# Kernel tuning notes

Measured on AMD Instinct MI355X. Metric: run time of the kernel, lower is better.

The kernel has to match this reference:

```python
import jax, jax.numpy as jnp
import numpy as np

N_HEAD = 12

def setup_inputs() -> dict:
    key = jax.random.key(0)
    ks = jax.random.split(key, 5)
    B, T, C = 4, 2048, 768
    x = jax.random.normal(ks[0], (B, T, C), dtype=jnp.float32)
    s_in = 1.0 / np.sqrt(C)
    W_qkv = jax.random.normal(ks[1], (C, 3 * C), dtype=jnp.float32) * s_in
    b_qkv = jnp.zeros((3 * C,), dtype=jnp.float32)
    W_proj = jax.random.normal(ks[2], (C, C), dtype=jnp.float32) * s_in
    b_proj = jnp.zeros((C,), dtype=jnp.float32)
    return {"x": x, "W_qkv": W_qkv, "b_qkv": b_qkv, "W_proj": W_proj, "b_proj": b_proj}


def reference(x, W_qkv, b_qkv, W_proj, b_proj):
    B, T, C = x.shape
    H = N_HEAD
    D = C // H  # head dim
    qkv = x @ W_qkv + b_qkv                      # [B,T,3C]
    q, k, v = jnp.split(qkv, 3, axis=-1)
    # [B,T,C] -> [B,H,T,D]
    q = q.reshape(B, T, H, D).transpose(0, 2, 1, 3)
    k = k.reshape(B, T, H, D).transpose(0, 2, 1, 3)
    v = v.reshape(B, T, H, D).transpose(0, 2, 1, 3)
    att = jnp.einsum("bhqd,bhkd->bhqk", q, k) / jnp.sqrt(jnp.asarray(D, x.dtype))
    causal = jnp.tril(jnp.ones((T, T), dtype=bool))
    att = jnp.where(causal, att, jnp.asarray(-jnp.inf, att.dtype))
    att = jax.nn.softmax(att, axis=-1)
    y = jnp.einsum("bhqk,bhkd->bhqd", att, v)    # [B,H,T,D]
    y = y.transpose(0, 2, 1, 3).reshape(B, T, C)
    return y @ W_proj + b_proj
```

## Files before the change

kernel.cpp:

```cpp
#include <hip/hip_runtime.h>
#include <hip/hip_bf16.h>

typedef __bf16 bf16x8 __attribute__((ext_vector_type(8)));
typedef float f32x4 __attribute__((ext_vector_type(4)));
typedef unsigned int u32x4 __attribute__((ext_vector_type(4)));
typedef unsigned int u32x2 __attribute__((ext_vector_type(2)));
typedef int i32x2 __attribute__((ext_vector_type(2)));
typedef unsigned short u16;
typedef unsigned long long u64;

__device__ __forceinline__ u16 f2bf(float f) {
  unsigned u = __builtin_bit_cast(unsigned, f);
  u += 0x7FFFu + ((u >> 16) & 1u);
  return (u16)(u >> 16);
}
__device__ __forceinline__ unsigned cvtpk(float a, float b) {
  float2 f; f.x = a; f.y = b;
  __hip_bfloat162 h = __float22bfloat162_rn(f);
  unsigned u;
  __builtin_memcpy(&u, &h, 4);
  return u;
}

__device__ __forceinline__ void plswap(unsigned &a, unsigned &b) {
  i32x2 r = __builtin_amdgcn_permlane32_swap((int)a, (int)b, false, false);
  a = (unsigned)r[0];
  b = (unsigned)r[1];
}

__device__ __forceinline__ void gll16(const u16* g, u16* l) {
  __builtin_amdgcn_global_load_lds(
      (const __attribute__((address_space(1))) unsigned int*)g,
      (__attribute__((address_space(3))) unsigned int*)l, 16, 0, 0);
}

__global__ void cast_x_kernel(const float* __restrict__ in, u16* __restrict__ out, int n4) {
  int i = blockIdx.x * blockDim.x + threadIdx.x;
  if (i >= n4) return;
  f32x4 v = *(const f32x4*)(in + (size_t)i * 4);
  u32x2 pk;
  pk[0] = cvtpk(v[0], v[1]);
  pk[1] = cvtpk(v[2], v[3]);
  *(u32x2*)(out + (size_t)i * 4) = pk;
}

__global__ void transpose_cast_kernel(const float* __restrict__ W, u16* __restrict__ WT, int K, int N) {
  __shared__ float tile[32][33];
  int c0 = blockIdx.x * 32, r0 = blockIdx.y * 32;
  int tx = threadIdx.x & 31, tg = threadIdx.x >> 5;
#pragma unroll
  for (int i = 0; i < 4; ++i) {
    int r = tg + i * 8;
    tile[r][tx] = W[(size_t)(r0 + r) * N + c0 + tx];
  }
  __syncthreads();
#pragma unroll
  for (int i = 0; i < 4; ++i) {
    int r = tg + i * 8;
    WT[(size_t)(c0 + r) * K + r0 + tx] = f2bf(tile[tx][r]);
  }
}

__global__ __launch_bounds__(256, 4) void gemm_qkv_kernel(
    const u16* __restrict__ A, const u16* __restrict__ BT, const float* __restrict__ bias,
    u16* __restrict__ Qb, u16* __restrict__ Kb, u16* __restrict__ Vt) {
  constexpr int K = 768;
  __shared__ u16 Asm[2][128 * 32];
  __shared__ u16 Bsm[2][128 * 32];
  const int tid = threadIdx.x;
  const int w = tid >> 6, lane = tid & 63;
  const int l15 = lane & 15, quad = lane >> 4;
  const int srow = tid >> 2, scol = (tid & 3) * 8;
  const int m0 = blockIdx.y * 128, n0 = blockIdx.x * 128;
  const u16* Ag = A + (size_t)(m0 + srow) * K + scol;
  const u16* Bg = BT + (size_t)(n0 + srow) * K + scol;
  const int mw = (w >> 1) * 64, nw = (w & 1) * 64;
  f32x4 acc[4][4];
#pragma unroll
  for (int i = 0; i < 4; ++i)
#pragma unroll
    for (int j = 0; j < 4; ++j) acc[i][j] = {0.f, 0.f, 0.f, 0.f};
  for (int k0 = 0; k0 < K; k0 += 64) {
    __syncthreads();
#pragma unroll
    for (int h = 0; h < 2; ++h)
#pragma unroll
      for (int rb = 0; rb < 2; ++rb) {
        gll16(Ag + (size_t)rb * 64 * K + k0 + h * 32, &Asm[h][(rb * 64 + w * 16) * 32]);
        gll16(Bg + (size_t)rb * 64 * K + k0 + h * 32, &Bsm[h][(rb * 64 + w * 16) * 32]);
      }
    __syncthreads();
#pragma unroll
    for (int h = 0; h < 2; ++h) {
      bf16x8 af[4], bfj[4];
#pragma unroll
      for (int i = 0; i < 4; ++i) af[i] = *(const bf16x8*)&Asm[h][(mw + i * 16 + l15) * 32 + quad * 8];
#pragma unroll
      for (int j = 0; j < 4; ++j) bfj[j] = *(const bf16x8*)&Bsm[h][(nw + j * 16 + l15) * 32 + quad * 8];
#pragma unroll
      for (int i = 0; i < 4; ++i)
#pragma unroll
        for (int j = 0; j < 4; ++j)
          acc[i][j] = __builtin_amdgcn_mfma_f32_16x16x32_bf16(af[i], bfj[j], acc[i][j], 0, 0, 0);
    }
  }
  const int sec = blockIdx.x / 6;
  const int nbase = n0 - sec * 768;
#pragma unroll
  for (int j = 0; j < 4; ++j) {
    const int nloc = nbase + nw + j * 16 + l15;
    const float bv = bias[sec * 768 + nloc];
    const int h = nloc >> 6, d = nloc & 63;
#pragma unroll
    for (int i = 0; i < 4; ++i) {
      const int m = m0 + mw + i * 16 + quad * 4;
      const int bb = m >> 11, trow = m & 2047;
      if (sec == 2) {
        u32x2 pk;
        pk[0] = cvtpk(acc[i][j][0] + bv, acc[i][j][1] + bv);
        pk[1] = cvtpk(acc[i][j][2] + bv, acc[i][j][3] + bv);
        *(u32x2*)(Vt + (size_t)((bb * 12 + h) * 64 + d) * 2048 + trow) = pk;
      } else {
        u16* dst = (sec == 0) ? Qb : Kb;
        const float scl = (sec == 0) ? 0.125f * 1.44269504f : 1.0f;
#pragma unroll
        for (int r = 0; r < 4; ++r)
          dst[(size_t)((bb * 12 + h) * 2048 + trow + r) * 64 + d] = f2bf((acc[i][j][r] + bv) * scl);
      }
    }
  }
}

__global__ __launch_bounds__(256, 4) void gemm_proj_kernel(
    const u16* __restrict__ A, const u16* __restrict__ BT, const float* __restrict__ bias,
    float* __restrict__ out) {
  constexpr int K = 768;
  __shared__ u16 Asm[2][64 * 32];
  __shared__ u16 Bsm[2][128 * 32];
  const int tid = threadIdx.x;
  const int w = tid >> 6, lane = tid & 63;
  const int l15 = lane & 15, quad = lane >> 4;
  const int srow = tid >> 2, scol = (tid & 3) * 8;
  const int m0 = blockIdx.y * 64, n0 = blockIdx.x * 128;
  const u16* Ag = A + (size_t)(m0 + srow) * K + scol;
  const u16* Bg = BT + (size_t)(n0 + srow) * K + scol;
  const int mw = (w >> 1) * 32, nw = (w & 1) * 64;
  f32x4 acc[2][4];
#pragma unroll
  for (int i = 0; i < 2; ++i)
#pragma unroll
    for (int j = 0; j < 4; ++j) acc[i][j] = {0.f, 0.f, 0.f, 0.f};
  for (int k0 = 0; k0 < K; k0 += 64) {
    __syncthreads();
#pragma unroll
    for (int h = 0; h < 2; ++h) {
      gll16(Ag + k0 + h * 32, &Asm[h][(w * 16) * 32]);
#pragma unroll
      for (int rb = 0; rb < 2; ++rb)
        gll16(Bg + (size_t)rb * 64 * K + k0 + h * 32, &Bsm[h][(rb * 64 + w * 16) * 32]);
    }
    __syncthreads();
#pragma unroll
    for (int h = 0; h < 2; ++h) {
      bf16x8 af[2], bfj[4];
#pragma unroll
      for (int i = 0; i < 2; ++i) af[i] = *(const bf16x8*)&Asm[h][(mw + i * 16 + l15) * 32 + quad * 8];
#pragma unroll
      for (int j = 0; j < 4; ++j) bfj[j] = *(const bf16x8*)&Bsm[h][(nw + j * 16 + l15) * 32 + quad * 8];
#pragma unroll
      for (int i = 0; i < 2; ++i)
#pragma unroll
        for (int j = 0; j < 4; ++j)
          acc[i][j] = __builtin_amdgcn_mfma_f32_16x16x32_bf16(af[i], bfj[j], acc[i][j], 0, 0, 0);
    }
  }
#pragma unroll
  for (int j = 0; j < 4; ++j) {
    const int n = n0 + nw + j * 16 + l15;
    const float bv = bias[n];
#pragma unroll
    for (int i = 0; i < 2; ++i) {
      const int m = m0 + mw + i * 16 + quad * 4;
#pragma unroll
      for (int r = 0; r < 4; ++r) out[(size_t)(m + r) * 768 + n] = acc[i][j][r] + bv;
    }
  }
}

__global__ __launch_bounds__(256) void attn_split_kernel(
    const u16* __restrict__ Qg, const u16* __restrict__ Kg, const u16* __restrict__ Vtg,
    u16* __restrict__ Yb, float* __restrict__ Opart, float* __restrict__ lpart) {
  constexpr int T = 2048, D = 64;
  constexpr int LDP = 72;
  constexpr float MBOUND = 20.0f;
  __shared__ u16 Ks[64 * LDP];
  __shared__ u16 VTs[64 * LDP];
  const int s = 79 - blockIdx.x;
  const int bh = blockIdx.y;
  int qt, c;
  if (s < 8) { qt = s; c = 0; }
  else if (s < 24) { qt = 8 + ((s - 8) >> 1); c = (s - 8) & 1; }
  else if (s < 48) { int u = s - 24; int q3 = u / 3; qt = 16 + q3; c = u - 3 * q3; }
  else { int u = s - 48; qt = 24 + (u >> 2); c = u & 3; }
  const int niter = min(8, qt + 1 - 8 * c);
  const int tid = threadIdx.x;
  const int w = tid >> 6, lane = tid & 63;
  const int l15 = lane & 15, quad = lane >> 4;
  const int srow = tid >> 2, scol = (tid & 3) * 16;
  const u16* Kp = Kg + (size_t)bh * T * D;
  const u16* VTp = Vtg + (size_t)bh * D * T;

  const int qq = qt * 64 + w * 16 + l15;
  const u16* qrow = Qg + ((size_t)bh * T + qq) * D;
  const bf16x8 qfa = *(const bf16x8*)(qrow + quad * 8);
  const bf16x8 qfb = *(const bf16x8*)(qrow + 32 + quad * 8);

  f32x4 o[4] = {{0,0,0,0},{0,0,0,0},{0,0,0,0},{0,0,0,0}};
  float lv = 0.f;

  int ktg = c * 8;
  u32x4 kA = *(const u32x4*)(Kp + (size_t)(ktg * 64 + srow) * D + scol);
  u32x4 kB = *(const u32x4*)(Kp + (size_t)(ktg * 64 + srow) * D + scol + 8);
  u32x4 vA = *(const u32x4*)(VTp + (size_t)srow * T + ktg * 64 + scol);
  u32x4 vB = *(const u32x4*)(VTp + (size_t)srow * T + ktg * 64 + scol + 8);

  for (int j = 0; j < niter; ++j) {
    ktg = c * 8 + j;
    __syncthreads();
    *(u32x4*)&Ks[srow * LDP + scol] = kA;
    *(u32x4*)&Ks[srow * LDP + scol + 8] = kB;
    {
      u32x2 t0; t0[0] = vA[0]; t0[1] = vA[1];
      u32x2 t1; t1[0] = vA[2]; t1[1] = vA[3];
      u32x2 t2; t2[0] = vB[0]; t2[1] = vB[1];
      u32x2 t3; t3[0] = vB[2]; t3[1] = vB[3];
      *(u32x2*)&VTs[srow * LDP + scol] = t0;
      *(u32x2*)&VTs[srow * LDP + scol + 8] = t1;
      *(u32x2*)&VTs[srow * LDP + scol + 4] = t2;
      *(u32x2*)&VTs[srow * LDP + scol + 12] = t3;
    }
    __syncthreads();
    if (j + 1 < niter) {
      const int k1 = (ktg + 1) * 64;
      kA = *(const u32x4*)(Kp + (size_t)(k1 + srow) * D + scol);
      kB = *(const u32x4*)(Kp + (size_t)(k1 + srow) * D + scol + 8);
      vA = *(const u32x4*)(VTp + (size_t)srow * T + k1 + scol);
      vB = *(const u32x4*)(VTp + (size_t)srow * T + k1 + scol + 8);
    }
    f32x4 sA[4];
#pragma unroll
    for (int t = 0; t < 4; ++t) sA[t] = {-MBOUND, -MBOUND, -MBOUND, -MBOUND};
#pragma unroll
    for (int t = 0; t < 4; ++t) {
      const bf16x8 kf0 = *(const bf16x8*)&Ks[(t * 16 + l15) * LDP + quad * 8];
      const bf16x8 kf1 = *(const bf16x8*)&Ks[(t * 16 + l15) * LDP + 32 + quad * 8];
      sA[t] = __builtin_amdgcn_mfma_f32_16x16x32_bf16(kf0, qfa, sA[t], 0, 0, 0);
      sA[t] = __builtin_amdgcn_mfma_f32_16x16x32_bf16(kf1, qfb, sA[t], 0, 0, 0);
    }
    if (ktg == qt) {
      const int k0 = ktg * 64;
#pragma unroll
      for (int t = 0; t < 4; ++t)
#pragma unroll
        for (int r = 0; r < 4; ++r)
          if (k0 + t * 16 + quad * 4 + r > qq) sA[t][r] = -1e30f;
    }
    unsigned W[4][2];
#pragma unroll
    for (int t = 0; t < 4; ++t) {
      float e0 = __builtin_amdgcn_exp2f(sA[t][0]);
      float e1 = __builtin_amdgcn_exp2f(sA[t][1]);
      float e2 = __builtin_amdgcn_exp2f(sA[t][2]);
      float e3 = __builtin_amdgcn_exp2f(sA[t][3]);
      lv += (e0 + e1) + (e2 + e3);
      W[t][0] = cvtpk(e0, e1);
      W[t][1] = cvtpk(e2, e3);
    }
    plswap(W[0][0], W[1][0]);
    plswap(W[0][1], W[1][1]);
    plswap(W[2][0], W[3][0]);
    plswap(W[2][1], W[3][1]);
    u32x4 paw; paw[0] = W[0][0]; paw[1] = W[0][1]; paw[2] = W[1][0]; paw[3] = W[1][1];
    u32x4 pbw; pbw[0] = W[2][0]; pbw[1] = W[2][1]; pbw[2] = W[3][0]; pbw[3] = W[3][1];
    const bf16x8 pa = __builtin_bit_cast(bf16x8, paw);
    const bf16x8 pb = __builtin_bit_cast(bf16x8, pbw);
#pragma unroll
    for (int t = 0; t < 4; ++t) {
      const bf16x8 vf0 = *(const bf16x8*)&VTs[(t * 16 + l15) * LDP + quad * 8];
      const bf16x8 vf1 = *(const bf16x8*)&VTs[(t * 16 + l15) * LDP + 32 + quad * 8];
      o[t] = __builtin_amdgcn_mfma_f32_16x16x32_bf16(vf0, pa, o[t], 0, 0, 0);
      o[t] = __builtin_amdgcn_mfma_f32_16x16x32_bf16(vf1, pb, o[t], 0, 0, 0);
    }
  }
  lv += __shfl_xor(lv, 16);
  lv += __shfl_xor(lv, 32);
  if (qt <= 7) {
    const float inv = 1.f / lv;
    const int bidx = bh / 12, hidx = bh % 12;
    u16* y = Yb + ((size_t)bidx * T + qq) * 768 + hidx * 64;
#pragma unroll
    for (int t = 0; t < 4; ++t) {
      u32x2 pk;
      pk[0] = cvtpk(o[t][0] * inv, o[t][1] * inv);
      pk[1] = cvtpk(o[t][2] * inv, o[t][3] * inv);
      *(u32x2*)(y + t * 16 + quad * 4) = pk;
    }
  } else {
    const size_t pidx = (size_t)bh * 80 + s;
    float* Op = Opart + pidx * 4096 + (size_t)(w * 16 + l15) * 64;
#pragma unroll
    for (int t = 0; t < 4; ++t) *(f32x4*)(Op + t * 16 + quad * 4) = o[t];
    if (quad == 0) lpart[pidx * 64 + w * 16 + l15] = lv;
  }
}

__global__ __launch_bounds__(256) void attn_combine_kernel(
    const float* __restrict__ Opart, const float* __restrict__ lpart, u16* __restrict__ Yb) {
  constexpr int T = 2048;
  const int qt = 8 + blockIdx.x;
  const int bh = blockIdx.y;
  const int nch = (qt < 16) ? 2 : (qt < 24) ? 3 : 4;
  const int off = (qt < 16) ? 8 + (qt - 8) * 2 : (qt < 24) ? 24 + (qt - 16) * 3 : 48 + (qt - 24) * 4;
  const size_t base = (size_t)bh * 80 + off;
  const int tid = threadIdx.x;
  const int q = tid >> 2, db = (tid & 3) * 16;
  f32x4 o[4] = {{0,0,0,0},{0,0,0,0},{0,0,0,0},{0,0,0,0}};
  float l = 0.f;
  for (int cc = 0; cc < nch; ++cc) {
    const float* Op = Opart + (base + cc) * 4096 + (size_t)q * 64 + db;
#pragma unroll
    for (int v = 0; v < 4; ++v) o[v] += *(const f32x4*)(Op + v * 4);
    l += lpart[(base + cc) * 64 + q];
  }
  const float inv = 1.f / l;
  const int bidx = bh / 12, hidx = bh % 12;
  u16* y = Yb + ((size_t)bidx * T + qt * 64 + q) * 768 + hidx * 64 + db;
  u32x4 pk;
  pk[0] = cvtpk(o[0][0] * inv, o[0][1] * inv);
  pk[1] = cvtpk(o[0][2] * inv, o[0][3] * inv);
  pk[2] = cvtpk(o[1][0] * inv, o[1][1] * inv);
  pk[3] = cvtpk(o[1][2] * inv, o[1][3] * inv);
  *(u32x4*)y = pk;
  pk[0] = cvtpk(o[2][0] * inv, o[2][1] * inv);
  pk[1] = cvtpk(o[2][2] * inv, o[2][3] * inv);
  pk[2] = cvtpk(o[3][0] * inv, o[3][1] * inv);
  pk[3] = cvtpk(o[3][2] * inv, o[3][3] * inv);
  *(u32x4*)(y + 8) = pk;
}

__global__ __launch_bounds__(256) void attn_kernel(
    const u16* __restrict__ Qg, const u16* __restrict__ Kg, const u16* __restrict__ Vtg,
    u16* __restrict__ Yb) {
  constexpr int T = 2048, D = 64;
  constexpr int LDP = 72;
  constexpr float MBOUND = 20.0f;
  __shared__ u16 Ks[64 * LDP];
  __shared__ u16 VTs[64 * LDP];
  __shared__ u16 Ps[4 * 32 * LDP];
  const int qb = 15 - blockIdx.x;
  const int bh = blockIdx.y;
  const int Q0 = qb * 128;
  const int bidx = bh / 12, hidx = bh % 12;
  const int tid = threadIdx.x;
  const int w = tid >> 6, lane = tid & 63;
  const int l15 = lane & 15, quad = lane >> 4;
  const int srow = tid >> 2, scol = (tid & 3) * 16;
  const u16* Kp = Kg + (size_t)bh * T * D;
  const u16* VTp = Vtg + (size_t)bh * D * T;
  u16* pw0 = &Ps[(w * 32) * LDP];
  u16* pw1 = &Ps[(w * 32 + 16) * LDP];
  const u16* qrow0 = Qg + ((size_t)bh * T + Q0 + w * 16 + l15) * D;
  const bf16x8 qf0a = *(const bf16x8*)(qrow0 + quad * 8);
  const bf16x8 qf0b = *(const bf16x8*)(qrow0 + 32 + quad * 8);
  const bf16x8 qf1a = *(const bf16x8*)(qrow0 + (size_t)64 * D + quad * 8);
  const bf16x8 qf1b = *(const bf16x8*)(qrow0 + (size_t)64 * D + 32 + quad * 8);
  const int qq0 = Q0 + w * 16 + l15, qq1 = qq0 + 64;
  f32x4 o0[4] = {{0,0,0,0},{0,0,0,0},{0,0,0,0},{0,0,0,0}};
  f32x4 o1[4] = {{0,0,0,0},{0,0,0,0},{0,0,0,0},{0,0,0,0}};
  float l0v = 0.f, l1v = 0.f;
  const int nkt = 2 * qb + 2;
  u32x4 kA = *(const u32x4*)(Kp + (size_t)srow * D + scol);
  u32x4 kB = *(const u32x4*)(Kp + (size_t)srow * D + scol + 8);
  u32x4 vA = *(const u32x4*)(VTp + (size_t)srow * T + scol);
  u32x4 vB = *(const u32x4*)(VTp + (size_t)srow * T + scol + 8);
  for (int kt = 0; kt < nkt; ++kt) {
    __syncthreads();
    *(u32x4*)&Ks[srow * LDP + scol] = kA;
    *(u32x4*)&Ks[srow * LDP + scol + 8] = kB;
    *(u32x4*)&VTs[srow * LDP + scol] = vA;
    *(u32x4*)&VTs[srow * LDP + scol + 8] = vB;
    __syncthreads();
    if (kt + 1 < nkt) {
      const int k1 = (kt + 1) * 64;
      kA = *(const u32x4*)(Kp + (size_t)(k1 + srow) * D + scol);
      kB = *(const u32x4*)(Kp + (size_t)(k1 + srow) * D + scol + 8);
      vA = *(const u32x4*)(VTp + (size_t)srow * T + k1 + scol);
      vB = *(const u32x4*)(VTp + (size_t)srow * T + k1 + scol + 8);
    }
    const int k0 = kt * 64;
    const bool g0a = (kt <= 2 * qb);
    f32x4 s0[4] = {{0,0,0,0},{0,0,0,0},{0,0,0,0},{0,0,0,0}};
    f32x4 s1[4] = {{0,0,0,0},{0,0,0,0},{0,0,0,0},{0,0,0,0}};
#pragma unroll
    for (int t = 0; t < 4; ++t) {
      const bf16x8 kf0 = *(const bf16x8*)&Ks[(t * 16 + l15) * LDP + quad * 8];
      const bf16x8 kf1 = *(const bf16x8*)&Ks[(t * 16 + l15) * LDP + 32 + quad * 8];
      s0[t] = __builtin_amdgcn_mfma_f32_16x16x32_bf16(kf0, qf0a, s0[t], 0, 0, 0);
      s0[t] = __builtin_amdgcn_mfma_f32_16x16x32_bf16(kf1, qf0b, s0[t], 0, 0, 0);
      s1[t] = __builtin_amdgcn_mfma_f32_16x16x32_bf16(kf0, qf1a, s1[t], 0, 0, 0);
      s1[t] = __builtin_amdgcn_mfma_f32_16x16x32_bf16(kf1, qf1b, s1[t], 0, 0, 0);
    }
    if (g0a) {
      if (kt == 2 * qb) {
#pragma unroll
        for (int t = 0; t < 4; ++t)
#pragma unroll
          for (int r = 0; r < 4; ++r)
            if (k0 + t * 16 + quad * 4 + r > qq0) s0[t][r] = -1e30f;
      }
#pragma unroll
      for (int t = 0; t < 4; ++t) {
        float e0 = __builtin_amdgcn_exp2f(s0[t][0] - MBOUND);
        float e1 = __builtin_amdgcn_exp2f(s0[t][1] - MBOUND);
        float e2 = __builtin_amdgcn_exp2f(s0[t][2] - MBOUND);
        float e3 = __builtin_amdgcn_exp2f(s0[t][3] - MBOUND);
        l0v += (e0 + e1) + (e2 + e3);
        u32x2 pk;
        pk[0] = cvtpk(e0, e1);
        pk[1] = cvtpk(e2, e3);
        *(u32x2*)&pw0[l15 * LDP + t * 16 + quad * 4] = pk;
      }
    }
    {
      if (kt == 2 * qb + 1) {
#pragma unroll
        for (int t = 0; t < 4; ++t)
#pragma unroll
          for (int r = 0; r < 4; ++r)
            if (k0 + t * 16 + quad * 4 + r > qq1) s1[t][r] = -1e30f;
      }
#pragma unroll
      for (int t = 0; t < 4; ++t) {
        float e0 = __builtin_amdgcn_exp2f(s1[t][0] - MBOUND);
        float e1 = __builtin_amdgcn_exp2f(s1[t][1] - MBOUND);
        float e2 = __builtin_amdgcn_exp2f(s1[t][2] - MBOUND);
        float e3 = __builtin_amdgcn_exp2f(s1[t][3] - MBOUND);
        l1v += (e0 + e1) + (e2 + e3);
        u32x2 pk;
        pk[0] = cvtpk(e0, e1);
        pk[1] = cvtpk(e2, e3);
        *(u32x2*)&pw1[l15 * LDP + t * 16 + quad * 4] = pk;
      }
    }
    const bf16x8 p0a = *(const bf16x8*)&pw0[l15 * LDP + quad * 8];
    const bf16x8 p0b = *(const bf16x8*)&pw0[l15 * LDP + 32 + quad * 8];
    const bf16x8 p1a = *(const bf16x8*)&pw1[l15 * LDP + quad * 8];
    const bf16x8 p1b = *(const bf16x8*)&pw1[l15 * LDP + 32 + quad * 8];
#pragma unroll
    for (int t = 0; t < 4; ++t) {
      const bf16x8 vf0 = *(const bf16x8*)&VTs[(t * 16 + l15) * LDP + quad * 8];
      const bf16x8 vf1 = *(const bf16x8*)&VTs[(t * 16 + l15) * LDP + 32 + quad * 8];
      if (g0a) {
        o0[t] = __builtin_amdgcn_mfma_f32_16x16x32_bf16(vf0, p0a, o0[t], 0, 0, 0);
        o0[t] = __builtin_amdgcn_mfma_f32_16x16x32_bf16(vf1, p0b, o0[t], 0, 0, 0);
      }
      o1[t] = __builtin_amdgcn_mfma_f32_16x16x32_bf16(vf0, p1a, o1[t], 0, 0, 0);
      o1[t] = __builtin_amdgcn_mfma_f32_16x16x32_bf16(vf1, p1b, o1[t], 0, 0, 0);
    }
  }
  l0v += __shfl_xor(l0v, 16); l0v += __shfl_xor(l0v, 32);
  l1v += __shfl_xor(l1v, 16); l1v += __shfl_xor(l1v, 32);
  const float inv0 = 1.f / l0v, inv1 = 1.f / l1v;
  u16* y0 = Yb + ((size_t)bidx * T + qq0) * 768 + hidx * 64;
  u16* y1 = Yb + ((size_t)bidx * T + qq1) * 768 + hidx * 64;
#pragma unroll
  for (int t = 0; t < 4; ++t) {
    u32x2 pk0, pk1;
    pk0[0] = cvtpk(o0[t][0] * inv0, o0[t][1] * inv0);
    pk0[1] = cvtpk(o0[t][2] * inv0, o0[t][3] * inv0);
    pk1[0] = cvtpk(o1[t][0] * inv1, o1[t][1] * inv1);
    pk1[1] = cvtpk(o1[t][2] * inv1, o1[t][3] * inv1);
    *(u32x2*)(y0 + t * 16 + quad * 4) = pk0;
    *(u32x2*)(y1 + t * 16 + quad * 4) = pk1;
  }
}

extern "C" void kernel_launch(void* const* d_in, const int* in_sizes, int n_in,
                              void* d_out, int out_size, void* d_ws, size_t ws_size,
                              hipStream_t stream) {
  const float* x = (const float*)d_in[0];
  const float* W_qkv = (const float*)d_in[1];
  const float* b_qkv = (const float*)d_in[2];
  const float* W_proj = (const float*)d_in[3];
  const float* b_proj = (const float*)d_in[4];
  float* out = (float*)d_out;

  constexpr size_t MC = (size_t)8192 * 768;
  u16* xb = (u16*)d_ws;
  u16* Qb = xb + MC;
  u16* Kb = Qb + MC;
  u16* Vt = Kb + MC;
  u16* Yb = Vt + MC;
  u16* WqkvT = Yb + MC;
  u16* WprojT = WqkvT + (size_t)2304 * 768;
  constexpr size_t BASE_U16 = 5 * MC + (size_t)2304 * 768 + (size_t)768 * 768;
  float* Opart = (float*)((u16*)d_ws + BASE_U16);
  float* lpart = Opart + (size_t)3840 * 4096;
  constexpr size_t NEED = BASE_U16 * 2 + ((size_t)3840 * 4096 + (size_t)3840 * 64) * 4;
  const bool use_split = (ws_size >= NEED);

  cast_x_kernel<<<6291456 / (4 * 256), 256, 0, stream>>>(x, xb, 6291456 / 4);
  transpose_cast_kernel<<<dim3(2304 / 32, 768 / 32), 256, 0, stream>>>(W_qkv, WqkvT, 768, 2304);
  transpose_cast_kernel<<<dim3(768 / 32, 768 / 32), 256, 0, stream>>>(W_proj, WprojT, 768, 768);
  gemm_qkv_kernel<<<dim3(18, 64), 256, 0, stream>>>(xb, WqkvT, b_qkv, Qb, Kb, Vt);
  if (use_split) {
    attn_split_kernel<<<dim3(80, 48), 256, 0, stream>>>(Qb, Kb, Vt, Yb, Opart, lpart);
    attn_combine_kernel<<<dim3(24, 48), 256, 0, stream>>>(Opart, lpart, Yb);
  } else {
    attn_kernel<<<dim3(16, 48), 256, 0, stream>>>(Qb, Kb, Vt, Yb);
  }
  gemm_proj_kernel<<<dim3(6, 128), 256, 0, stream>>>(Yb, WprojT, b_proj, out);
}
```

Before: 231.4 us.

## Double-buffer QKV and projection GEMM K-loops to overlap global loads with MFMA

Both GEMM kernels change from a load-all-then-compute loop over 64-wide K chunks to a two-stage ping-pong pipeline over 32-wide K slices. The next slice's global-to-LDS loads are issued before computing the current one, using manual vmcnt waits and raw s_barrier. The aim is to hide global memory latency behind MFMA work instead of stalling on a full barrier each iteration. In exchange there are twice as many barriers per K, and correctness now depends on the hand-counted vmcnt values matching the number of outstanding loads.

Result: no change. 229.2 us (-0.9%).

```diff
diff --git a/kernel.cpp b/kernel.cpp
--- a/kernel.cpp
+++ b/kernel.cpp
@@ -8,6 +8,9 @@
 typedef int i32x2 __attribute__((ext_vector_type(2)));
 typedef unsigned short u16;
 typedef unsigned long long u64;
+
+#define WAITVM(n) asm volatile("s_waitcnt vmcnt(" #n ")" ::: "memory")
+#define SBAR() asm volatile("s_barrier" ::: "memory")
 
 __device__ __forceinline__ u16 f2bf(float f) {
   unsigned u = __builtin_bit_cast(unsigned, f);
@@ -65,6 +68,7 @@
     const u16* __restrict__ A, const u16* __restrict__ BT, const float* __restrict__ bias,
     u16* __restrict__ Qb, u16* __restrict__ Kb, u16* __restrict__ Vt) {
   constexpr int K = 768;
+  constexpr int NS = K / 32;
   __shared__ u16 Asm[2][128 * 32];
   __shared__ u16 Bsm[2][128 * 32];
   const int tid = threadIdx.x;
@@ -80,30 +84,37 @@
   for (int i = 0; i < 4; ++i)
 #pragma unroll
     for (int j = 0; j < 4; ++j) acc[i][j] = {0.f, 0.f, 0.f, 0.f};
-  for (int k0 = 0; k0 < K; k0 += 64) {
-    __syncthreads();
-#pragma unroll
-    for (int h = 0; h < 2; ++h)
-#pragma unroll
-      for (int rb = 0; rb < 2; ++rb) {
-        gll16(Ag + (size_t)rb * 64 * K + k0 + h * 32, &Asm[h][(rb * 64 + w * 16) * 32]);
-        gll16(Bg + (size_t)rb * 64 * K + k0 + h * 32, &Bsm[h][(rb * 64 + w * 16) * 32]);
-      }
-    __syncthreads();
-#pragma unroll
-    for (int h = 0; h < 2; ++h) {
-      bf16x8 af[4], bfj[4];
-#pragma unroll
-      for (int i = 0; i < 4; ++i) af[i] = *(const bf16x8*)&Asm[h][(mw + i * 16 + l15) * 32 + quad * 8];
-#pragma unroll
-      for (int j = 0; j < 4; ++j) bfj[j] = *(const bf16x8*)&Bsm[h][(nw + j * 16 + l15) * 32 + quad * 8];
-#pragma unroll
-      for (int i = 0; i < 4; ++i)
-#pragma unroll
-        for (int j = 0; j < 4; ++j)
-          acc[i][j] = __builtin_amdgcn_mfma_f32_16x16x32_bf16(af[i], bfj[j], acc[i][j], 0, 0, 0);
-    }
-  }
+
+  auto STAGE = [&](int buf, int ks) {
+    const u16* a = Ag + ks * 32;
+    const u16* b = Bg + ks * 32;
+#pragma unroll
+    for (int rb = 0; rb < 2; ++rb) {
+      gll16(a + (size_t)rb * 64 * K, &Asm[buf][(rb * 64 + w * 16) * 32]);
+      gll16(b + (size_t)rb * 64 * K, &Bsm[buf][(rb * 64 + w * 16) * 32]);
+    }
+  };
+  auto COMPUTE = [&](int buf) {
+    bf16x8 af[4], bfj[4];
+#pragma unroll
+    for (int i = 0; i < 4; ++i) af[i] = *(const bf16x8*)&Asm[buf][(mw + i * 16 + l15) * 32 + quad * 8];
+#pragma unroll
+    for (int j = 0; j < 4; ++j) bfj[j] = *(const bf16x8*)&Bsm[buf][(nw + j * 16 + l15) * 32 + quad * 8];
+#pragma unroll
+    for (int i = 0; i < 4; ++i)
+#pragma unroll
+      for (int j = 0; j < 4; ++j)
+        acc[i][j] = __builtin_amdgcn_mfma_f32_16x16x32_bf16(af[i], bfj[j], acc[i][j], 0, 0, 0);
+  };
+
+  STAGE(0, 0);
+  for (int s = 0; s + 2 < NS; s += 2) {
+    STAGE(1, s + 1); WAITVM(4); SBAR(); COMPUTE(0); SBAR();
+    STAGE(0, s + 2); WAITVM(4); SBAR(); COMPUTE(1); SBAR();
+  }
+  STAGE(1, NS - 1); WAITVM(4); SBAR(); COMPUTE(0);
+  WAITVM(0); SBAR(); COMPUTE(1);
+
   const int sec = blockIdx.x / 6;
   const int nbase = n0 - sec * 768;
 #pragma unroll
@@ -135,6 +146,7 @@
     const u16* __restrict__ A, const u16* __restrict__ BT, const float* __restrict__ bias,
     float* __restrict__ out) {
   constexpr int K = 768;
+  constexpr int NS = K / 32;
   __shared__ u16 Asm[2][64 * 32];
   __shared__ u16 Bsm[2][128 * 32];
   const int tid = threadIdx.x;
@@ -150,30 +162,36 @@
   for (int i = 0; i < 2; ++i)
 #pragma unroll
     for (int j = 0; j < 4; ++j) acc[i][j] = {0.f, 0.f, 0.f, 0.f};
-  for (int k0 = 0; k0 < K; k0 += 64) {
-    __syncthreads();
-#pragma unroll
-    for (int h = 0; h < 2; ++h) {
-      gll16(Ag + k0 + h * 32, &Asm[h][(w * 16) * 32]);
-#pragma unroll
-      for (int rb = 0; rb < 2; ++rb)
-        gll16(Bg + (size_t)rb * 64 * K + k0 + h * 32, &Bsm[h][(rb * 64 + w * 16) * 32]);
-    }
-    __syncthreads();
-#pragma unroll
-    for (int h = 0; h < 2; ++h) {
-      bf16x8 af[2], bfj[4];
-#pragma unroll
-      for (int i = 0; i < 2; ++i) af[i] = *(const bf16x8*)&Asm[h][(mw + i * 16 + l15) * 32 + quad * 8];
-#pragma unroll
-      for (int j = 0; j < 4; ++j) bfj[j] = *(const bf16x8*)&Bsm[h][(nw + j * 16 + l15) * 32 + quad * 8];
-#pragma unroll
-      for (int i = 0; i < 2; ++i)
-#pragma unroll
-        for (int j = 0; j < 4; ++j)
-          acc[i][j] = __builtin_amdgcn_mfma_f32_16x16x32_bf16(af[i], bfj[j], acc[i][j], 0, 0, 0);
-    }
-  }
+
+  auto STAGE = [&](int buf, int ks) {
+    const u16* a = Ag + ks * 32;
+    const u16* b = Bg + ks * 32;
+    gll16(a, &Asm[buf][(w * 16) * 32]);
+#pragma unroll
+    for (int rb = 0; rb < 2; ++rb)
+      gll16(b + (size_t)rb * 64 * K, &Bsm[buf][(rb * 64 + w * 16) * 32]);
+  };
+  auto COMPUTE = [&](int buf) {
+    bf16x8 af[2], bfj[4];
+#pragma unroll
+    for (int i = 0; i < 2; ++i) af[i] = *(const bf16x8*)&Asm[buf][(mw + i * 16 + l15) * 32 + quad * 8];
+#pragma unroll
+    for (int j = 0; j < 4; ++j) bfj[j] = *(const bf16x8*)&Bsm[buf][(nw + j * 16 + l15) * 32 + quad * 8];
+#pragma unroll
+    for (int i = 0; i < 2; ++i)
+#pragma unroll
+      for (int j = 0; j < 4; ++j)
+        acc[i][j] = __builtin_amdgcn_mfma_f32_16x16x32_bf16(af[i], bfj[j], acc[i][j], 0, 0, 0);
+  };
+
+  STAGE(0, 0);
+  for (int s = 0; s + 2 < NS; s += 2) {
+    STAGE(1, s + 1); WAITVM(3); SBAR(); COMPUTE(0); SBAR();
+    STAGE(0, s + 2); WAITVM(3); SBAR(); COMPUTE(1); SBAR();
+  }
+  STAGE(1, NS - 1); WAITVM(3); SBAR(); COMPUTE(0);
+  WAITVM(0); SBAR(); COMPUTE(1);
+
 #pragma unroll
   for (int j = 0; j < 4; ++j) {
     const int n = n0 + nw + j * 16 + l15;
```
